# Optimization experiments

Measured on AMD Instinct MI355X. Metric: run time of the kernel, lower is better.

Reference implementation:

```python
import jax, jax.numpy as jnp
import numpy as np
from jax import lax

WINDOW_SIZE = 11
SIGMA = 1.5


def _gaussian_window(window_size, channel, dtype):
    x = np.arange(window_size)
    g = np.exp(-((x - window_size // 2) ** 2) / (2.0 * SIGMA ** 2))
    g = g / g.sum()
    w2d = np.outer(g, g).astype(np.float32)  # [k,k]
    # depthwise kernel, OIHW with I=1, O=channel
    w = np.broadcast_to(w2d[None, None], (channel, 1, window_size, window_size))
    return jnp.asarray(w, dtype=dtype)


def _dwconv(x, window, channel, pad):
    # x: [B,C,H,W]; depthwise conv with 'same' padding
    return lax.conv_general_dilated(
        x, window, window_strides=(1, 1),
        padding=[(pad, pad), (pad, pad)],
        feature_group_count=channel,
        dimension_numbers=("NCHW", "OIHW", "NCHW"))


def setup_inputs() -> dict:
    key = jax.random.key(0)
    k1, k2, k3 = jax.random.split(key, 3)
    B, C, H, W = 16, 3, 512, 1024
    img1 = jax.random.uniform(k1, (B, C, H, W), dtype=jnp.float32)
    img2 = jax.random.uniform(k2, (B, C, H, W), dtype=jnp.float32)
    mask_pos = jax.random.randint(k3, (B,), 0, 768, dtype=jnp.int64)
    return {"img1": img1, "img2": img2, "mask_pos": mask_pos, "mask_width": 256}


def reference(img1, img2, mask_pos, mask_width):
    B, C, H, W = img1.shape
    w = int(mask_width)
    # clamp start like torch: max(0, min(pos, W - w))
    starts = jnp.clip(mask_pos.astype(jnp.int32), 0, W - w)

    def crop(im, s):
        return lax.dynamic_slice(im, (0, 0, s), (C, H, w))

    m1 = jax.vmap(crop)(img1, starts)  # [B,C,H,w]
    m2 = jax.vmap(crop)(img2, starts)

    L = 1.0  # source returns 1.0 on both branches when val_range is None
    pad = WINDOW_SIZE // 2
    window = _gaussian_window(WINDOW_SIZE, C, m1.dtype)

    mu1 = _dwconv(m1, window, C, pad)
    mu2 = _dwconv(m2, window, C, pad)
    mu1_sq = mu1 * mu1
    mu2_sq = mu2 * mu2
    mu1_mu2 = mu1 * mu2
    sigma1_sq = _dwconv(m1 * m1, window, C, pad) - mu1_sq
    sigma2_sq = _dwconv(m2 * m2, window, C, pad) - mu2_sq
    sigma12 = _dwconv(m1 * m2, window, C, pad) - mu1_mu2

    C1 = (0.01 * L) ** 2
    C2 = (0.03 * L) ** 2
    eps = 1e-5
    ssim_map = ((2.0 * mu1_mu2 + C1) * (2.0 * sigma12 + C2) + eps) / (
        (mu1_sq + mu2_sq + C1) * (sigma1_sq + sigma2_sq + C2) + eps)
    return 1.0 - ssim_map.mean()
```

## Files before the change

kernel.cpp:

```cpp
#include <hip/hip_runtime.h>

#define B_     16
#define C_     3
#define H_     512
#define W_     1024
#define MW     256
#define RS     16
#define NSTRIP 32
#define NIN    (RS + 10)

#define FENCE() __builtin_amdgcn_wave_barrier()

__global__ __launch_bounds__(256) void ssim_main(const float* __restrict__ img1,
                                                 const float* __restrict__ img2,
                                                 const int*   __restrict__ mask_pos,
                                                 float*       __restrict__ accum) {
    constexpr float G[11] = {
        0.00102838f, 0.00759876f, 0.03600077f, 0.10936070f, 0.21300553f,
        0.26601173f, 0.21300553f, 0.10936070f, 0.03600077f, 0.00759876f,
        0.00102838f };

    __shared__ float2 rowbuf[4][2][80];
    __shared__ float  blksum[4];

    const int tid  = threadIdx.x;
    const int w    = tid >> 6;
    const int lane = tid & 63;

    const int d     = blockIdx.x;
    const int xcd   = d & 7;
    const int q     = d >> 3;
    const int bc    = xcd * 6 + (q >> 5);
    const int strip = q & 31;
    const int b     = bc / 3;

    int s0 = mask_pos[b];
    s0 = min(max(s0, 0), W_ - MW);

    const float* __restrict__ p1 = img1 + (size_t)bc * (H_ * W_);
    const float* __restrict__ p2 = img2 + (size_t)bc * (H_ * W_);

    const int y0  = strip * RS;
    const int sx0 = w << 6;
    const int cxm = sx0 - 5 + lane;
    const int cxh = sx0 + 59 + lane;
    const bool vm = (cxm >= 0) && (cxm < MW);
    const bool vh = (lane < 10) && (cxh < MW);
    const int gxm = s0 + cxm;
    const int gxh = s0 + cxh;

    float pa0, pb0, pa1, pb1;
    auto loadrow = [&](int r) {
        pa0 = pb0 = pa1 = pb1 = 0.f;
        if (r >= 0 && r < H_) {
            const int ro = r * W_;
            if (vm) { pa0 = p1[ro + gxm]; pb0 = p2[ro + gxm]; }
            if (vh) { pa1 = p1[ro + gxh]; pb1 = p2[ro + gxh]; }
        }
    };

    float acc[11][4];
    #pragma unroll
    for (int s = 0; s < 11; ++s)
        #pragma unroll
        for (int f = 0; f < 4; ++f) acc[s][f] = 0.f;

    float psum = 0.f;
    int cur = 0;

    auto dorow = [&](int i, int sl) {
        const bool notlast = (i + 1 < NIN);

        if (notlast) loadrow(y0 - 4 + i);

        float su = 0.f, sv = 0.f, suu = 0.f, svv = 0.f;
        #pragma unroll
        for (int t = 0; t < 11; ++t) {
            const float2 q2 = rowbuf[w][cur][lane + t];
            const float gu = G[t] * q2.x;
            const float gv = G[t] * q2.y;
            su += gu;
            sv += gv;
            suu = fmaf(gu, q2.x, suu);
            svv = fmaf(gv, q2.y, svv);
        }

        #pragma unroll
        for (int m = 0; m < 11; ++m) {
            const int s = (sl + m) % 11;
            const float gw = G[10 - m];
            acc[s][0] = fmaf(gw, su,  acc[s][0]);
            acc[s][1] = fmaf(gw, sv,  acc[s][1]);
            acc[s][2] = fmaf(gw, suu, acc[s][2]);
            acc[s][3] = fmaf(gw, svv, acc[s][3]);
        }

        if (i >= 10) {
            const float mup = acc[sl][0], mum = acc[sl][1];
            const float Suu = acc[sl][2], Svv = acc[sl][3];
            const float A  = mup * mup, Bq = mum * mum;
            const float mu_sq_sum = 0.5f * (A + Bq);
            const float mu_cross2 = 0.5f * (A - Bq);
            const float e_sum     = 0.5f * (Suu + Svv);
            const float e_cross2  = 0.5f * (Suu - Svv);
            const float sig_sum = e_sum - mu_sq_sum;
            const float sig12_2 = e_cross2 - mu_cross2;
            const float num = (mu_cross2 + 1e-4f) * (sig12_2 + 9e-4f) + 1e-5f;
            const float den = (mu_sq_sum + 1e-4f) * (sig_sum + 9e-4f) + 1e-5f;
            psum += __fdividef(num, den);
        }
        #pragma unroll
        for (int f = 0; f < 4; ++f) acc[sl][f] = 0.f;

        if (notlast) {
            rowbuf[w][cur ^ 1][lane] = make_float2(pa0 + pb0, pa0 - pb0);
            if (lane < 10)
                rowbuf[w][cur ^ 1][64 + lane] = make_float2(pa1 + pb1, pa1 - pb1);
        }
        cur ^= 1;
        FENCE();
    };

    loadrow(y0 - 5);
    rowbuf[w][0][lane] = make_float2(pa0 + pb0, pa0 - pb0);
    if (lane < 10) rowbuf[w][0][64 + lane] = make_float2(pa1 + pb1, pa1 - pb1);
    FENCE();

    for (int ii = 0; ii < 22; ii += 11) {
        #pragma unroll
        for (int j = 0; j < 11; ++j) dorow(ii + j, j);
    }
    #pragma unroll
    for (int j = 0; j < 4; ++j) dorow(22 + j, j);

    #pragma unroll
    for (int off = 32; off > 0; off >>= 1) psum += __shfl_xor(psum, off, 64);
    if (lane == 0) blksum[w] = psum;
    __syncthreads();
    if (tid == 0) {
        atomicAdd(accum, blksum[0] + blksum[1] + blksum[2] + blksum[3]);
    }
}

__global__ void ssim_final(const float* __restrict__ accum, float* __restrict__ out) {
    out[0] = 1.0f - accum[0] * (1.0f / 6291456.0f);
}

extern "C" void kernel_launch(void* const* d_in, const int* in_sizes, int n_in,
                              void* d_out, int out_size, void* d_ws, size_t ws_size,
                              hipStream_t stream) {
    const float* img1 = (const float*)d_in[0];
    const float* img2 = (const float*)d_in[1];
    const int*   pos  = (const int*)d_in[2];
    float* out = (float*)d_out;
    float* acc = (float*)d_ws;

    hipMemsetAsync(acc, 0, sizeof(float), stream);

    ssim_main<<<B_ * C_ * NSTRIP, 256, 0, stream>>>(img1, img2, pos, acc);
    ssim_final<<<1, 1, 0, stream>>>(acc, out);
}
```

Before: 46.83 us.

## Prefetch rows two ahead and fold final reduction into main kernel

Global row loads now run two rows ahead using two register sets (A/B) that alternate by parity, so load latency has more compute to hide behind. The separate finalize kernel is removed: the last block to finish, found through an atomic counter, writes the output. This saves one kernel launch but adds register pressure and a threadfence plus atomic per block.

```diff
diff --git a/kernel.cpp b/kernel.cpp
--- a/kernel.cpp
+++ b/kernel.cpp
@@ -8,13 +8,16 @@
 #define RS     16
 #define NSTRIP 32
 #define NIN    (RS + 10)
+#define NBLK   (B_ * C_ * NSTRIP)
 
 #define FENCE() __builtin_amdgcn_wave_barrier()
 
 __global__ __launch_bounds__(256) void ssim_main(const float* __restrict__ img1,
                                                  const float* __restrict__ img2,
                                                  const int*   __restrict__ mask_pos,
-                                                 float*       __restrict__ accum) {
+                                                 float*        __restrict__ accum,
+                                                 unsigned int* __restrict__ cnt,
+                                                 float*        __restrict__ out) {
     constexpr float G[11] = {
         0.00102838f, 0.00759876f, 0.03600077f, 0.10936070f, 0.21300553f,
         0.26601173f, 0.21300553f, 0.10936070f, 0.03600077f, 0.00759876f,
@@ -49,14 +52,32 @@
     const int gxm = s0 + cxm;
     const int gxh = s0 + cxh;
 
-    float pa0, pb0, pa1, pb1;
-    auto loadrow = [&](int r) {
-        pa0 = pb0 = pa1 = pb1 = 0.f;
+    float Aa0, Ab0, Aa1, Ab1;
+    float Ba0, Bb0, Ba1, Bb1;
+
+    auto loadA = [&](int r) {
+        Aa0 = Ab0 = Aa1 = Ab1 = 0.f;
         if (r >= 0 && r < H_) {
             const int ro = r * W_;
-            if (vm) { pa0 = p1[ro + gxm]; pb0 = p2[ro + gxm]; }
-            if (vh) { pa1 = p1[ro + gxh]; pb1 = p2[ro + gxh]; }
+            if (vm) { Aa0 = p1[ro + gxm]; Ab0 = p2[ro + gxm]; }
+            if (vh) { Aa1 = p1[ro + gxh]; Ab1 = p2[ro + gxh]; }
         }
+    };
+    auto loadB = [&](int r) {
+        Ba0 = Bb0 = Ba1 = Bb1 = 0.f;
+        if (r >= 0 && r < H_) {
+            const int ro = r * W_;
+            if (vm) { Ba0 = p1[ro + gxm]; Bb0 = p2[ro + gxm]; }
+            if (vh) { Ba1 = p1[ro + gxh]; Bb1 = p2[ro + gxh]; }
+        }
+    };
+    auto storeA = [&]() {
+        rowbuf[w][0][lane] = make_float2(Aa0 + Ab0, Aa0 - Ab0);
+        if (lane < 10) rowbuf[w][0][64 + lane] = make_float2(Aa1 + Ab1, Aa1 - Ab1);
+    };
+    auto storeB = [&]() {
+        rowbuf[w][1][lane] = make_float2(Ba0 + Bb0, Ba0 - Bb0);
+        if (lane < 10) rowbuf[w][1][64 + lane] = make_float2(Ba1 + Bb1, Ba1 - Bb1);
     };
 
     float acc[11][4];
@@ -66,17 +87,17 @@
         for (int f = 0; f < 4; ++f) acc[s][f] = 0.f;
 
     float psum = 0.f;
-    int cur = 0;
 
-    auto dorow = [&](int i, int sl) {
-        const bool notlast = (i + 1 < NIN);
-
-        if (notlast) loadrow(y0 - 4 + i);
+    auto dorow = [&](int i, int sl, int par) {
+        if (i + 2 < NIN) {
+            if (par == 0) loadA(y0 - 3 + i);
+            else          loadB(y0 - 3 + i);
+        }
 
         float su = 0.f, sv = 0.f, suu = 0.f, svv = 0.f;
         #pragma unroll
         for (int t = 0; t < 11; ++t) {
-            const float2 q2 = rowbuf[w][cur][lane + t];
+            const float2 q2 = rowbuf[w][par][lane + t];
             const float gu = G[t] * q2.x;
             const float gv = G[t] * q2.y;
             su += gu;
@@ -112,26 +133,22 @@
         #pragma unroll
         for (int f = 0; f < 4; ++f) acc[sl][f] = 0.f;
 
-        if (notlast) {
-            rowbuf[w][cur ^ 1][lane] = make_float2(pa0 + pb0, pa0 - pb0);
-            if (lane < 10)
-                rowbuf[w][cur ^ 1][64 + lane] = make_float2(pa1 + pb1, pa1 - pb1);
+        if (i + 1 < NIN) {
+            if (par == 0) storeB();
+            else          storeA();
         }
-        cur ^= 1;
         FENCE();
     };
 
-    loadrow(y0 - 5);
-    rowbuf[w][0][lane] = make_float2(pa0 + pb0, pa0 - pb0);
-    if (lane < 10) rowbuf[w][0][64 + lane] = make_float2(pa1 + pb1, pa1 - pb1);
+    loadA(y0 - 5);
+    loadB(y0 - 4);
+    storeA();
     FENCE();
 
-    for (int ii = 0; ii < 22; ii += 11) {
-        #pragma unroll
-        for (int j = 0; j < 11; ++j) dorow(ii + j, j);
-    }
     #pragma unroll
-    for (int j = 0; j < 4; ++j) dorow(22 + j, j);
+    for (int j = 0; j < 22; ++j) dorow(j, j % 11, j & 1);
+    #pragma unroll
+    for (int j = 0; j < 4; ++j) dorow(22 + j, j, j & 1);
 
     #pragma unroll
     for (int off = 32; off > 0; off >>= 1) psum += __shfl_xor(psum, off, 64);
@@ -139,11 +156,13 @@
     __syncthreads();
     if (tid == 0) {
         atomicAdd(accum, blksum[0] + blksum[1] + blksum[2] + blksum[3]);
+        __threadfence();
+        const unsigned int done = atomicAdd(cnt, 1u);
+        if (done == NBLK - 1) {
+            const float tot = atomicAdd(accum, 0.f);
+            out[0] = 1.0f - tot * (1.0f / 6291456.0f);
+        }
     }
-}
-
-__global__ void ssim_final(const float* __restrict__ accum, float* __restrict__ out) {
-    out[0] = 1.0f - accum[0] * (1.0f / 6291456.0f);
 }
 
 extern "C" void kernel_launch(void* const* d_in, const int* in_sizes, int n_in,
@@ -152,11 +171,11 @@
     const float* img1 = (const float*)d_in[0];
     const float* img2 = (const float*)d_in[1];
     const int*   pos  = (const int*)d_in[2];
-    float* out = (float*)d_out;
-    float* acc = (float*)d_ws;
+    float*        acc = (float*)d_ws;
+    unsigned int* cnt = (unsigned int*)((char*)d_ws + 4);
 
-    hipMemsetAsync(acc, 0, sizeof(float), stream);
+    hipMemsetAsync(d_ws, 0, 8, stream);
 
-    ssim_main<<<B_ * C_ * NSTRIP, 256, 0, stream>>>(img1, img2, pos, acc);
-    ssim_final<<<1, 1, 0, stream>>>(acc, out);
+    ssim_main<<<NBLK, 256, 0, stream>>>(img1, img2, pos, acc, cnt,
+                                        (float*)d_out);
 }
```

Result: slower. 129.4 us (+176.3%).
